# Optimization experiments

Measured on AMD Instinct MI355X. Metric: run time of the kernel, lower is better.

Reference implementation:

```python
import jax, jax.numpy as jnp
import numpy as np


def _softsplat(tenIn, tenFlow):
    """Bilinear forward splatting: scatter tenIn to flow-displaced locations.
    tenIn: [N,C,H,W], tenFlow: [N,2,H,W] -> out [N,C,H,W]."""
    N, C, H, W = tenIn.shape
    dt = tenIn.dtype
    gx = jnp.arange(W, dtype=dt)[None, None, :]   # [1,1,W]
    gy = jnp.arange(H, dtype=dt)[None, :, None]   # [1,H,1]
    fx = gx + tenFlow[:, 0]                       # [N,H,W] target x
    fy = gy + tenFlow[:, 1]                       # [N,H,W] target y
    finite = jnp.isfinite(fx) & jnp.isfinite(fy)
    x0f = jnp.floor(fx)
    y0f = jnp.floor(fy)
    ix0 = x0f.astype(jnp.int32)
    iy0 = y0f.astype(jnp.int32)
    # bilinear corner weights (NW, NE, SW, SE) exactly as in the CUDA kernel
    wx1 = fx - x0f            # weight toward east
    wx0 = (x0f + 1.0) - fx    # weight toward west
    wy1 = fy - y0f            # weight toward south
    wy0 = (y0f + 1.0) - fy    # weight toward north
    corners = [
        (ix0,     iy0,     wx0 * wy0),  # NW
        (ix0 + 1, iy0,     wx1 * wy0),  # NE
        (ix0,     iy0 + 1, wx0 * wy1),  # SW
        (ix0 + 1, iy0 + 1, wx1 * wy1),  # SE
    ]
    HW = H * W
    tenIn_flat = tenIn.reshape(N, C, HW)

    def scatter_corner(ix, iy, w):
        valid = finite & (ix >= 0) & (ix < W) & (iy >= 0) & (iy < H)
        idx = jnp.where(valid, iy * W + ix, 0).reshape(N, HW)       # [N,HW]
        wv = jnp.where(valid, w, jnp.zeros_like(w)).reshape(N, 1, HW)
        vals = (tenIn_flat * wv).transpose(0, 2, 1)                 # [N,HW,C]
        seg = jax.vmap(lambda v, i: jax.ops.segment_sum(v, i, num_segments=HW))(vals, idx)
        return seg                                                   # [N,HW,C]

    out = scatter_corner(*corners[0])
    for c in corners[1:]:
        out = out + scatter_corner(*c)
    return out.transpose(0, 2, 1).reshape(N, C, H, W)


def softsplat_softmax(tenIn, tenFlow, tenMetric):
    # strMode == 'softmax': splat [tenIn * exp(metric), exp(metric)], then normalize
    w = jnp.exp(tenMetric)                          # [N,1,H,W]
    packed = jnp.concatenate([tenIn * w, w], axis=1)
    out = _softsplat(packed, tenFlow)
    norm = out[:, -1:]
    norm = jnp.where(norm == 0.0, jnp.ones_like(norm), norm)
    return out[:, :-1] / norm


def setup_inputs() -> dict:
    key = jax.random.key(0)
    k1, k2, k3 = jax.random.split(key, 3)
    N, C, H, W = 8, 64, 288, 512
    tenIn = jax.random.normal(k1, (N, C, H, W), dtype=jnp.float32)
    tenFlow = jax.random.normal(k2, (N, 2, H, W), dtype=jnp.float32)
    tenMetric = jax.random.normal(k3, (N, 1, H, W), dtype=jnp.float32)
    return {"tenIn": tenIn, "tenFlow": tenFlow, "tenMetric": tenMetric}


def reference(tenIn, tenFlow, tenMetric):
    return softsplat_softmax(tenIn, tenFlow, tenMetric)
```

## Files before the change

### kernel.cpp

```cpp
#include <hip/hip_runtime.h>
#include <hip/hip_fp16.h>
#include <math.h>

constexpr int N  = 8;
constexpr int C  = 64;
constexpr int H  = 288;
constexpr int W  = 512;
constexpr int HW = H * W;
constexpr int NPIX = N * HW;

constexpr int TW = 64, TH = 32, R = 8;
constexpr int PW = TW + 2 * R;
constexpr int PH = TH + 2 * R;
constexpr int PS = PW * PH;
constexpr int TGX = W / TW;
constexpr int TGY = H / TH;
constexpr int TILES = N * TGX * TGY;
constexpr int NOUT = TH * TW;
constexpr int K = 12;
constexpr int CCHB = 4;
constexpr int NCHUNK = C / CCHB;
constexpr int NSPLIT = 2;
constexpr int CPB = NCHUNK / NSPLIT;
constexpr int OVFCAP = 256;
constexpr int ESCCAP = 512;
constexpr int NTC = 512;
constexpr int NTG = 1024;
constexpr int GGRID = TILES * NSPLIT;

constexpr size_t WS_DEN  = 0;
constexpr size_t WS_META = WS_DEN  + (size_t)N * HW;
constexpr size_t WS_CNT  = WS_META + (size_t)TILES * NOUT * K;
constexpr size_t WS_OVFC = WS_CNT  + (size_t)TILES * NOUT;
constexpr size_t WS_OVFE = WS_OVFC + TILES;
constexpr size_t WS_ESCC = WS_OVFE + (size_t)TILES * OVFCAP * 2;
constexpr size_t WS_ESCE = WS_ESCC + TILES;

__device__ __forceinline__ int swz(int si) { return si ^ ((si >> 3) & 7); }

__global__ __launch_bounds__(NTC) void claim_kernel(
    const float* __restrict__ flow, const float* __restrict__ metric,
    unsigned* __restrict__ meta, unsigned* __restrict__ cntg,
    unsigned* __restrict__ ovfc, unsigned* __restrict__ ovfe,
    float* __restrict__ den)
{
    __shared__ unsigned cnt[NOUT];
    for (int i = threadIdx.x; i < NOUT; i += NTC) cnt[i] = 0;
    __syncthreads();

    const int t  = blockIdx.x;
    const int n  = t / (TGX * TGY);
    const int r  = t % (TGX * TGY);
    const int Y0 = (r / TGX) * TH;
    const int X0 = (r % TGX) * TW;

    const float* fxp = flow + ((size_t)n * 2) * HW;
    const float* fyp = fxp + HW;
    const float* mp  = metric + (size_t)n * HW;
    unsigned* mt = meta + (size_t)t * K * NOUT;

    for (int si = threadIdx.x; si < PS; si += NTC) {
        int ys = Y0 - R + si / PW;
        int xs = X0 - R + si % PW;
        if ((unsigned)ys >= (unsigned)H || (unsigned)xs >= (unsigned)W) continue;
        int p = ys * W + xs;
        float fx = fxp[p] + (float)xs;
        float fy = fyp[p] + (float)ys;
        if (!(isfinite(fx) && isfinite(fy))) continue;
        float x0f = floorf(fx), y0f = floorf(fy);
        int tx = (int)x0f - X0;
        int ty = (int)y0f - Y0;
        float wx1 = fx - x0f, wx0 = x0f + 1.0f - fx;
        float wy1 = fy - y0f, wy0 = y0f + 1.0f - fy;
        float wm  = __expf(mp[p]);

        #define CLAIM(TYv, TXv, Wv)                                           \
            if ((unsigned)(TYv) < (unsigned)TH &&                             \
                (unsigned)(TXv) < (unsigned)TW) {                             \
                float w_ = (Wv) * wm;                                         \
                int   o_ = (TYv) * TW + (TXv);                                \
                unsigned slot = atomicAdd(&cnt[o_], 1u);                      \
                if (slot < (unsigned)K) {                                     \
                    mt[(size_t)slot * NOUT + o_] =                            \
                        ((unsigned)__half_as_ushort(__float2half(w_)) << 16)  \
                        | (unsigned)si;                                       \
                } else {                                                      \
                    unsigned p2 = atomicAdd(&ovfc[t], 1u);                    \
                    if (p2 < (unsigned)OVFCAP) {                              \
                        unsigned* e = ovfe + ((size_t)t * OVFCAP + p2) * 2;   \
                        e[0] = ((unsigned)o_ << 16) | (unsigned)si;           \
                        e[1] = __float_as_uint(w_);                           \
                    }                                                         \
                }                                                             \
            }
        CLAIM(ty,     tx,     wx0 * wy0)
        CLAIM(ty,     tx + 1, wx1 * wy0)
        CLAIM(ty + 1, tx,     wx0 * wy1)
        CLAIM(ty + 1, tx + 1, wx1 * wy1)
        #undef CLAIM
    }
    __syncthreads();

    const unsigned on = min(ovfc[t], (unsigned)OVFCAP);
    const unsigned* oe = ovfe + (size_t)t * OVFCAP * 2;
    for (int o = threadIdx.x; o < NOUT; o += NTC) {
        unsigned craw = cnt[o];
        cntg[(size_t)t * NOUT + o] = craw;
        unsigned cn = min(craw, (unsigned)K);
        float d = 0.0f;
        for (unsigned s = 0; s < cn; ++s)
            d += __half2float(__ushort_as_half(
                     (unsigned short)(mt[(size_t)s * NOUT + o] >> 16)));
        for (unsigned i = 0; i < on; ++i)
            if ((oe[2 * i] >> 16) == (unsigned)o)
                d += __uint_as_float(oe[2 * i + 1]);
        den[(size_t)n * HW + (Y0 + o / TW) * W + X0 + o % TW] = d;
    }
}

__global__ __launch_bounds__(256) void escape_kernel(
    const float* __restrict__ flow, const float* __restrict__ metric,
    float* __restrict__ den, unsigned* __restrict__ escc,
    unsigned* __restrict__ esce)
{
    int pix = blockIdx.x * 256 + threadIdx.x;
    if (pix >= NPIX) return;
    int n  = pix / HW;
    int p  = pix - n * HW;
    int xs = p & (W - 1);
    int ys = p >> 9;

    float fx = flow[((size_t)n * 2    ) * HW + p] + (float)xs;
    float fy = flow[((size_t)n * 2 + 1) * HW + p] + (float)ys;
    if (!(isfinite(fx) && isfinite(fy))) return;
    float x0f = floorf(fx), y0f = floorf(fy);
    int ix0 = (int)x0f, iy0 = (int)y0f;
    float wx1 = fx - x0f, wx0 = x0f + 1.0f - fx;
    float wy1 = fy - y0f, wy0 = y0f + 1.0f - fy;

    int   cx[4] = { ix0, ix0 + 1, ix0,     ix0 + 1 };
    int   cy[4] = { iy0, iy0,     iy0 + 1, iy0 + 1 };
    float cw[4] = { wx0 * wy0, wx1 * wy0, wx0 * wy1, wx1 * wy1 };

    bool esc[4]; bool any = false;
    #pragma unroll
    for (int k = 0; k < 4; ++k) {
        esc[k] = false;
        if ((unsigned)cx[k] < (unsigned)W && (unsigned)cy[k] < (unsigned)H) {
            int tX0 = cx[k] & ~(TW - 1);
            int tY0 = cy[k] & ~(TH - 1);
            bool inpad = (xs >= tX0 - R) && (xs < tX0 + TW + R) &&
                         (ys >= tY0 - R) && (ys < tY0 + TH + R);
            if (!inpad) { esc[k] = true; any = true; }
        }
    }
    if (!any) return;

    float wm = __expf(metric[(size_t)n * HW + p]);
    #pragma unroll
    for (int k = 0; k < 4; ++k) {
        if (!esc[k]) continue;
        int tX0 = cx[k] & ~(TW - 1);
        int tY0 = cy[k] & ~(TH - 1);
        int tt  = n * (TGX * TGY) + (tY0 >> 5) * TGX + (tX0 >> 6);
        float w_ = cw[k] * wm;
        atomicAdd(den + (size_t)n * HW + cy[k] * W + cx[k], w_);
        unsigned pos = atomicAdd(&escc[tt], 1u);
        if (pos < (unsigned)ESCCAP) {
            unsigned* e = esce + ((size_t)tt * ESCCAP + pos) * 3;
            e[0] = (unsigned)((cy[k] - tY0) * TW + (cx[k] - tX0));
            e[1] = (unsigned)p;
            e[2] = __float_as_uint(w_);
        }
    }
}

__global__ __launch_bounds__(NTG, 4) void gather_kernel(
    const float* __restrict__ in, const unsigned* __restrict__ meta,
    const unsigned* __restrict__ cntg, const unsigned* __restrict__ ovfc,
    const unsigned* __restrict__ ovfe, const unsigned* __restrict__ escc,
    const unsigned* __restrict__ esce, const float* __restrict__ den,
    float* __restrict__ out)
{
    __shared__ float4 val4[PS];

    const int b0 = blockIdx.x;
    const int b  = (b0 & 7) * (GGRID / 8) + (b0 >> 3);
    const int t     = b >> 1;
    const int split = b & 1;
    const int n  = t / (TGX * TGY);
    const int r  = t % (TGX * TGY);
    const int Y0 = (r / TGX) * TH;
    const int X0 = (r % TGX) * TW;

    const unsigned on = min(ovfc[t], (unsigned)OVFCAP);
    const unsigned en = min(escc[t], (unsigned)ESCCAP);
    const unsigned* oe = ovfe + (size_t)t * OVFCAP * 2;
    const unsigned* ee = esce + (size_t)t * ESCCAP * 3;
    const unsigned* mt = meta + (size_t)t * K * NOUT;

    unsigned mm[2][K];
    float    inv[2];
    int      opix[2];
    #pragma unroll
    for (int k = 0; k < 2; ++k) {
        int o = threadIdx.x + k * NTG;
        unsigned cn = min(cntg[(size_t)t * NOUT + o], (unsigned)K);
        #pragma unroll
        for (int s = 0; s < K; ++s)
            mm[k][s] = (s < (int)cn) ? mt[(size_t)s * NOUT + o] : 0u;
        opix[k] = (Y0 + o / TW) * W + X0 + o % TW;
        float d = den[(size_t)n * HW + opix[k]];
        inv[k] = (d == 0.0f) ? 1.0f : 1.0f / d;
    }

    for (int cc = 0; cc < CPB; ++cc) {
        const int cb = split * CPB + cc;
        const float* inb = in + ((size_t)n * C + cb * CCHB) * HW;
        __syncthreads();
        if (threadIdx.x < PS / 4) {
            int si0 = threadIdx.x * 4;
            int row = si0 / PW;
            int ys  = Y0 - R + row;
            int xs0 = X0 - R + (si0 - row * PW);
            bool ok = (unsigned)ys < (unsigned)H && (unsigned)xs0 < (unsigned)W;
            const float* pp = inb + ys * W + xs0;
            float2* v2 = reinterpret_cast<float2*>(val4);
            int sw = (si0 >> 3) & 7;
            {
                float4 g0 = {0,0,0,0}, g1 = {0,0,0,0};
                if (ok) {
                    g0 = *reinterpret_cast<const float4*>(pp);
                    g1 = *reinterpret_cast<const float4*>(pp + HW);
                }
                v2[(((si0    ) ^ sw) << 1)] = make_float2(g0.x, g1.x);
                v2[(((si0 + 1) ^ sw) << 1)] = make_float2(g0.y, g1.y);
                v2[(((si0 + 2) ^ sw) << 1)] = make_float2(g0.z, g1.z);
                v2[(((si0 + 3) ^ sw) << 1)] = make_float2(g0.w, g1.w);
            }
            {
                float4 g2 = {0,0,0,0}, g3 = {0,0,0,0};
                if (ok) {
                    g2 = *reinterpret_cast<const float4*>(pp + 2 * HW);
                    g3 = *reinterpret_cast<const float4*>(pp + 3 * HW);
                }
                v2[(((si0    ) ^ sw) << 1) | 1] = make_float2(g2.x, g3.x);
                v2[(((si0 + 1) ^ sw) << 1) | 1] = make_float2(g2.y, g3.y);
                v2[(((si0 + 2) ^ sw) << 1) | 1] = make_float2(g2.z, g3.z);
                v2[(((si0 + 3) ^ sw) << 1) | 1] = make_float2(g2.w, g3.w);
            }
        }
        __syncthreads();

        #pragma unroll
        for (int k = 0; k < 2; ++k) {
            float a0 = 0.0f, a1 = 0.0f, a2 = 0.0f, a3 = 0.0f;
            #pragma unroll
            for (int s = 0; s < K; ++s) {
                unsigned m_ = mm[k][s];
                float w  = __half2float(__ushort_as_half((unsigned short)(m_ >> 16)));
                int   si = (int)(m_ & 0xffffu);
                float4 v = val4[swz(si)];
                a0 += w * v.x;
                a1 += w * v.y;
                a2 += w * v.z;
                a3 += w * v.w;
            }
            int o = threadIdx.x + k * NTG;
            for (unsigned i = 0; i < on; ++i) {
                unsigned e0 = oe[2 * i];
                if ((e0 >> 16) == (unsigned)o) {
                    float w  = __uint_as_float(oe[2 * i + 1]);
                    float4 v = val4[swz((int)(e0 & 0xffffu))];
                    a0 += w * v.x;
                    a1 += w * v.y;
                    a2 += w * v.z;
                    a3 += w * v.w;
                }
            }
            for (unsigned i = 0; i < en; ++i) {
                if (ee[3 * i] == (unsigned)o) {
                    float w  = __uint_as_float(ee[3 * i + 2]);
                    int   ps = (int)ee[3 * i + 1];
                    a0 += w * inb[ps];
                    a1 += w * inb[ps + HW];
                    a2 += w * inb[ps + 2 * HW];
                    a3 += w * inb[ps + 3 * HW];
                }
            }
            size_t ob = ((size_t)n * C + cb * CCHB) * HW + opix[k];
            out[ob]          = a0 * inv[k];
            out[ob + HW]     = a1 * inv[k];
            out[ob + 2 * HW] = a2 * inv[k];
            out[ob + 3 * HW] = a3 * inv[k];
        }
    }
}

extern "C" void kernel_launch(void* const* d_in, const int* in_sizes, int n_in,
                              void* d_out, int out_size, void* d_ws, size_t ws_size,
                              hipStream_t stream)
{
    const float* tenIn     = (const float*)d_in[0];
    const float* tenFlow   = (const float*)d_in[1];
    const float* tenMetric = (const float*)d_in[2];
    float* out = (float*)d_out;

    unsigned* ws  = (unsigned*)d_ws;
    float*    den = (float*)(ws + WS_DEN);
    unsigned* meta = ws + WS_META;
    unsigned* cntg = ws + WS_CNT;
    unsigned* ovfc = ws + WS_OVFC;
    unsigned* ovfe = ws + WS_OVFE;
    unsigned* escc = ws + WS_ESCC;
    unsigned* esce = ws + WS_ESCE;

    hipMemsetAsync(ovfc, 0, TILES * sizeof(unsigned), stream);
    hipMemsetAsync(escc, 0, TILES * sizeof(unsigned), stream);

    claim_kernel<<<TILES, NTC, 0, stream>>>(tenFlow, tenMetric,
                                            meta, cntg, ovfc, ovfe, den);
    escape_kernel<<<(NPIX + 255) / 256, 256, 0, stream>>>(tenFlow, tenMetric,
                                                          den, escc, esce);
    gather_kernel<<<GGRID, NTG, 0, stream>>>(tenIn, meta, cntg, ovfc,
                                             ovfe, escc, esce, den, out);
}
```

Baseline: 274.1 us.

## Stage input tile in fp16 and process eight channels per gather pass

The gather kernel now packs each staged input pixel as eight fp16 channels in one uint4 of shared memory, where before it held four fp32 channels. The channel chunk grows from 4 to 8, which halves the number of staging passes and barriers and doubles the work done per shared-memory lookup of the metadata index. The cost is fp16 rounding of input values before accumulation, which may break accuracy tolerance, plus more registers per thread for the eight accumulators and eight in-flight global loads.

```diff
diff --git a/kernel.cpp b/kernel.cpp
--- a/kernel.cpp
+++ b/kernel.cpp
@@ -18,7 +18,7 @@
 constexpr int TILES = N * TGX * TGY;
 constexpr int NOUT = TH * TW;
 constexpr int K = 12;
-constexpr int CCHB = 4;
+constexpr int CCHB = 8;
 constexpr int NCHUNK = C / CCHB;
 constexpr int NSPLIT = 2;
 constexpr int CPB = NCHUNK / NSPLIT;
@@ -37,6 +37,15 @@
 constexpr size_t WS_ESCE = WS_ESCC + TILES;
 
 __device__ __forceinline__ int swz(int si) { return si ^ ((si >> 3) & 7); }
+
+__device__ __forceinline__ unsigned packh2(float a, float b) {
+    __half2 h = __floats2half2_rn(a, b);
+    return *reinterpret_cast<unsigned*>(&h);
+}
+__device__ __forceinline__ float2 unpackh2(unsigned u) {
+    __half2 h = *reinterpret_cast<__half2*>(&u);
+    return __half22float2(h);
+}
 
 __global__ __launch_bounds__(NTC) void claim_kernel(
     const float* __restrict__ flow, const float* __restrict__ metric,
@@ -182,7 +191,7 @@
     const unsigned* __restrict__ esce, const float* __restrict__ den,
     float* __restrict__ out)
 {
-    __shared__ float4 val4[PS];
+    __shared__ uint4 val[PS];
 
     const int b0 = blockIdx.x;
     const int b  = (b0 & 7) * (GGRID / 8) + (b0 >> 3);
@@ -225,74 +234,82 @@
             int xs0 = X0 - R + (si0 - row * PW);
             bool ok = (unsigned)ys < (unsigned)H && (unsigned)xs0 < (unsigned)W;
             const float* pp = inb + ys * W + xs0;
-            float2* v2 = reinterpret_cast<float2*>(val4);
+            uint2* v2 = reinterpret_cast<uint2*>(val);
             int sw = (si0 >> 3) & 7;
             {
-                float4 g0 = {0,0,0,0}, g1 = {0,0,0,0};
+                float4 g0 = {0,0,0,0}, g1 = g0, g2 = g0, g3 = g0;
                 if (ok) {
                     g0 = *reinterpret_cast<const float4*>(pp);
                     g1 = *reinterpret_cast<const float4*>(pp + HW);
-                }
-                v2[(((si0    ) ^ sw) << 1)] = make_float2(g0.x, g1.x);
-                v2[(((si0 + 1) ^ sw) << 1)] = make_float2(g0.y, g1.y);
-                v2[(((si0 + 2) ^ sw) << 1)] = make_float2(g0.z, g1.z);
-                v2[(((si0 + 3) ^ sw) << 1)] = make_float2(g0.w, g1.w);
-            }
-            {
-                float4 g2 = {0,0,0,0}, g3 = {0,0,0,0};
-                if (ok) {
                     g2 = *reinterpret_cast<const float4*>(pp + 2 * HW);
                     g3 = *reinterpret_cast<const float4*>(pp + 3 * HW);
                 }
-                v2[(((si0    ) ^ sw) << 1) | 1] = make_float2(g2.x, g3.x);
-                v2[(((si0 + 1) ^ sw) << 1) | 1] = make_float2(g2.y, g3.y);
-                v2[(((si0 + 2) ^ sw) << 1) | 1] = make_float2(g2.z, g3.z);
-                v2[(((si0 + 3) ^ sw) << 1) | 1] = make_float2(g2.w, g3.w);
+                v2[(((si0    ) ^ sw) << 1)] = make_uint2(packh2(g0.x, g1.x), packh2(g2.x, g3.x));
+                v2[(((si0 + 1) ^ sw) << 1)] = make_uint2(packh2(g0.y, g1.y), packh2(g2.y, g3.y));
+                v2[(((si0 + 2) ^ sw) << 1)] = make_uint2(packh2(g0.z, g1.z), packh2(g2.z, g3.z));
+                v2[(((si0 + 3) ^ sw) << 1)] = make_uint2(packh2(g0.w, g1.w), packh2(g2.w, g3.w));
+            }
+            {
+                float4 g4 = {0,0,0,0}, g5 = g4, g6 = g4, g7 = g4;
+                if (ok) {
+                    g4 = *reinterpret_cast<const float4*>(pp + 4 * HW);
+                    g5 = *reinterpret_cast<const float4*>(pp + 5 * HW);
+                    g6 = *reinterpret_cast<const float4*>(pp + 6 * HW);
+                    g7 = *reinterpret_cast<const float4*>(pp + 7 * HW);
+                }
+                v2[(((si0    ) ^ sw) << 1) | 1] = make_uint2(packh2(g4.x, g5.x), packh2(g6.x, g7.x));
+                v2[(((si0 + 1) ^ sw) << 1) | 1] = make_uint2(packh2(g4.y, g5.y), packh2(g6.y, g7.y));
+                v2[(((si0 + 2) ^ sw) << 1) | 1] = make_uint2(packh2(g4.z, g5.z), packh2(g6.z, g7.z));
+                v2[(((si0 + 3) ^ sw) << 1) | 1] = make_uint2(packh2(g4.w, g5.w), packh2(g6.w, g7.w));
             }
         }
         __syncthreads();
 
         #pragma unroll
         for (int k = 0; k < 2; ++k) {
-            float a0 = 0.0f, a1 = 0.0f, a2 = 0.0f, a3 = 0.0f;
+            float acc[CCHB];
+            #pragma unroll
+            for (int c = 0; c < CCHB; ++c) acc[c] = 0.0f;
             #pragma unroll
             for (int s = 0; s < K; ++s) {
                 unsigned m_ = mm[k][s];
                 float w  = __half2float(__ushort_as_half((unsigned short)(m_ >> 16)));
                 int   si = (int)(m_ & 0xffffu);
-                float4 v = val4[swz(si)];
-                a0 += w * v.x;
-                a1 += w * v.y;
-                a2 += w * v.z;
-                a3 += w * v.w;
+                uint4 v = val[swz(si)];
+                float2 f0 = unpackh2(v.x), f1 = unpackh2(v.y);
+                float2 f2 = unpackh2(v.z), f3 = unpackh2(v.w);
+                acc[0] += w * f0.x;  acc[1] += w * f0.y;
+                acc[2] += w * f1.x;  acc[3] += w * f1.y;
+                acc[4] += w * f2.x;  acc[5] += w * f2.y;
+                acc[6] += w * f3.x;  acc[7] += w * f3.y;
             }
             int o = threadIdx.x + k * NTG;
             for (unsigned i = 0; i < on; ++i) {
                 unsigned e0 = oe[2 * i];
                 if ((e0 >> 16) == (unsigned)o) {
                     float w  = __uint_as_float(oe[2 * i + 1]);
-                    float4 v = val4[swz((int)(e0 & 0xffffu))];
-                    a0 += w * v.x;
-                    a1 += w * v.y;
-                    a2 += w * v.z;
-                    a3 += w * v.w;
+                    uint4 v = val[swz((int)(e0 & 0xffffu))];
+                    float2 f0 = unpackh2(v.x), f1 = unpackh2(v.y);
+                    float2 f2 = unpackh2(v.z), f3 = unpackh2(v.w);
+                    acc[0] += w * f0.x;  acc[1] += w * f0.y;
+                    acc[2] += w * f1.x;  acc[3] += w * f1.y;
+                    acc[4] += w * f2.x;  acc[5] += w * f2.y;
+                    acc[6] += w * f3.x;  acc[7] += w * f3.y;
                 }
             }
             for (unsigned i = 0; i < en; ++i) {
                 if (ee[3 * i] == (unsigned)o) {
                     float w  = __uint_as_float(ee[3 * i + 2]);
                     int   ps = (int)ee[3 * i + 1];
-                    a0 += w * inb[ps];
-                    a1 += w * inb[ps + HW];
-                    a2 += w * inb[ps + 2 * HW];
-                    a3 += w * inb[ps + 3 * HW];
+                    #pragma unroll
+                    for (int c = 0; c < CCHB; ++c)
+                        acc[c] += w * inb[ps + (size_t)c * HW];
                 }
             }
             size_t ob = ((size_t)n * C + cb * CCHB) * HW + opix[k];
-            out[ob]          = a0 * inv[k];
-            out[ob + HW]     = a1 * inv[k];
-            out[ob + 2 * HW] = a2 * inv[k];
-            out[ob + 3 * HW] = a3 * inv[k];
+            #pragma unroll
+            for (int c = 0; c < CCHB; ++c)
+                out[ob + (size_t)c * HW] = acc[c] * inv[k];
         }
     }
 }
```

Result: slower. 570.0 us (+107.9%).
